# Performance work log

Hardware: AMD Instinct MI355X
Metric: run time of the kernel (lower is better)

Reference implementation:

```python
import jax, jax.numpy as jnp
import numpy as np

N_NODES = 50000
N_EDGES = 1600000
HID = 128
N_LAYERS = 3
N_GRAPHS = 64
LN_EPS = 1e-5


def setup_inputs() -> dict:
    key = jax.random.key(0)
    ks = jax.random.split(key, 8)
    x = jax.random.normal(ks[0], (N_NODES, HID), dtype=jnp.float32)
    edge_index = jax.random.randint(ks[1], (2, N_EDGES), 0, N_NODES)
    batch = jnp.sort(jax.random.randint(ks[2], (N_NODES,), 0, N_GRAPHS))
    s = 1.0 / np.sqrt(HID)
    Wn = jax.random.normal(ks[3], (N_LAYERS, HID, HID), dtype=jnp.float32) * s   # lin_l (neighbors)
    bn = jnp.zeros((N_LAYERS, HID), dtype=jnp.float32)                           # lin_l bias
    Wr = jax.random.normal(ks[4], (N_LAYERS, HID, HID), dtype=jnp.float32) * s   # lin_r (root), no bias
    gamma = jnp.ones((N_LAYERS, HID), dtype=jnp.float32)
    beta = jnp.zeros((N_LAYERS, HID), dtype=jnp.float32)
    return {"x": x, "Wn": Wn, "bn": bn, "Wr": Wr, "gamma": gamma, "beta": beta,
            "edge_index": edge_index, "batch": batch}


def _layer_norm(h, g, b):
    mu = jnp.mean(h, axis=-1, keepdims=True)
    var = jnp.mean((h - mu) ** 2, axis=-1, keepdims=True)
    return (h - mu) * jax.lax.rsqrt(var + LN_EPS) * g + b


def reference(x, Wn, bn, Wr, gamma, beta, edge_index, batch):
    src, dst = edge_index[0], edge_index[1]
    N = x.shape[0]
    # in-degree for mean aggregation (clamped to avoid div-by-zero for isolated nodes)
    deg = jax.ops.segment_sum(jnp.ones((src.shape[0],), x.dtype), dst, num_segments=N)
    inv_deg = 1.0 / jnp.maximum(deg, 1.0)
    for l in range(N_LAYERS):
        # SAGEConv: lin_l(mean_neighbor) + lin_r(x)
        agg = jax.ops.segment_sum(x[src], dst, num_segments=N) * inv_deg[:, None]
        h = agg @ Wn[l] + bn[l] + x @ Wr[l]
        h = _layer_norm(h, gamma[l], beta[l])
        x = jax.nn.relu(h)  # dropout is identity in eval mode
    node_emb = x
    cnt = jax.ops.segment_sum(jnp.ones((N,), x.dtype), batch, num_segments=N_GRAPHS)
    graph_emb = jax.ops.segment_sum(node_emb, batch, num_segments=N_GRAPHS) / jnp.maximum(cnt, 1.0)[:, None]
    return graph_emb, node_emb
```

## Files before the change

kernel.cpp:

```cpp
#include <hip/hip_runtime.h>

#define N_NODES 50000
#define N_EDGES 1600000
#define HID     128
#define N_GRAPHS 64

#define HB 200
#define EPB (N_EDGES / HB)
#define HWORDS 12500
#define NPP 12500
#define CWPP (NPP / 4)
#define NGRP 8
#define SPG (HB / NGRP)

#define WS_DEG   0u
#define WS_BSUM  50000u
#define WS_BOFF  50256u
#define WS_OFFS  50512u
#define WS_INVD  100512u
#define WS_CSR   150512u
#define WS_XB_B  1750512u
#define WS_GSUM  (WS_XB_B + 2500000u)
#define WS_XB_A  4950512u
#define WS_WP    8150512u
#define WS_END   8199664u

typedef __attribute__((ext_vector_type(8))) short short8;
typedef __attribute__((ext_vector_type(4))) float floatx4;

__device__ __forceinline__ float bf_lo(unsigned u) { return __uint_as_float(u << 16); }
__device__ __forceinline__ float bf_hi(unsigned u) { return __uint_as_float(u & 0xffff0000u); }
__device__ __forceinline__ unsigned bf_rn(float f) {
    unsigned u = __float_as_uint(f);
    unsigned r = ((u >> 16) & 1u) + 0x7fffu;
    return (u + r) >> 16;
}
__device__ __forceinline__ unsigned bf_pack(float lo, float hi) {
    return bf_rn(lo) | (bf_rn(hi) << 16);
}

__global__ __launch_bounds__(256) void k_prep(const float4* __restrict__ x, uint2* __restrict__ o,
                                              const float* __restrict__ Wn, const float* __restrict__ Wr,
                                              uint4* __restrict__ wp, const int* __restrict__ ei,
                                              unsigned* __restrict__ hist) {
    __shared__ unsigned sh[HWORDS];
    if (blockIdx.x < 6250) {
        int i = blockIdx.x * 256 + threadIdx.x;
        float4 v = x[i];
        uint2 r;
        r.x = bf_pack(v.x, v.y);
        r.y = bf_pack(v.z, v.w);
        o[i] = r;
    } else if (blockIdx.x < 6298) {
        int idx = (blockIdx.x - 6250) * 256 + threadIdx.x;
        int layer = idx >> 12;
        int rem = idx & 4095;
        int kb = rem >> 9;
        int n = (rem >> 2) & 127;
        int quad = rem & 3;
        float v[8];
#pragma unroll
        for (int j = 0; j < 8; j++) {
            int k = kb * 32 + quad * 8 + j;
            v[j] = (k < 128) ? Wn[layer * 16384 + k * 128 + n]
                             : Wr[layer * 16384 + (k - 128) * 128 + n];
        }
        uint4 r;
        r.x = bf_pack(v[0], v[1]);
        r.y = bf_pack(v[2], v[3]);
        r.z = bf_pack(v[4], v[5]);
        r.w = bf_pack(v[6], v[7]);
        wp[idx] = r;
    } else {
        const int hb = blockIdx.x - 6298;
        for (int i = threadIdx.x; i < HWORDS; i += 256) sh[i] = 0;
        __syncthreads();
        const int e0 = hb * EPB;
        for (int i = threadIdx.x; i < EPB; i += 256) {
            int d = __builtin_nontemporal_load(ei + N_EDGES + e0 + i);
            atomicAdd(&sh[d >> 2], 1u << ((d & 3) << 3));
        }
        __syncthreads();
        unsigned* hp = hist + (size_t)hb * HWORDS;
        for (int i = threadIdx.x; i < HWORDS; i += 256) hp[i] = sh[i];
    }
}


__global__ __launch_bounds__(256) void k_scanb1(unsigned* __restrict__ hist, unsigned* __restrict__ gsum) {
    int wb = blockIdx.x % 49;
    int g = blockIdx.x / 49;
    int w = wb * 256 + threadIdx.x;
    if (w >= HWORDS) return;
    size_t base = (size_t)(g * SPG) * HWORDS + w;
    unsigned run = 0;
#pragma unroll 5
    for (int b = 0; b < SPG; ++b) {
        unsigned u = hist[base + (size_t)b * HWORDS];
        hist[base + (size_t)b * HWORDS] = run;
        run += u;
    }
    gsum[(size_t)g * HWORDS + w] = run;
}

__global__ __launch_bounds__(256) void k_scanb2(unsigned* __restrict__ gsum, int* __restrict__ deg,
                                                int* __restrict__ bsum) {
    int w = blockIdx.x * 256 + threadIdx.x;
    int mysum = 0;
    if (w < HWORDS) {
        unsigned run = 0;
#pragma unroll
        for (int g = 0; g < NGRP; ++g) {
            unsigned u = gsum[(size_t)g * HWORDS + w];
            gsum[(size_t)g * HWORDS + w] = run;
            run += u;
        }
#pragma unroll
        for (int k = 0; k < 4; ++k) {
            int d = (int)((run >> (k << 3)) & 0xffu);
            deg[4 * w + k] = d;
            mysum += d;
        }
    }
    __shared__ int s[256];
    s[threadIdx.x] = mysum;
    __syncthreads();
    for (int d = 128; d > 0; d >>= 1) {
        if (threadIdx.x < d) s[threadIdx.x] += s[threadIdx.x + d];
        __syncthreads();
    }
    if (threadIdx.x == 0) bsum[blockIdx.x] = s[0];
}

__global__ __launch_bounds__(256) void k_offsets(const int* __restrict__ deg, const int* __restrict__ bsum,
                                                 int* __restrict__ offs, float* __restrict__ invdeg) {
    __shared__ int sb[64], sb0[64];
    __shared__ int s[256];
    int b = blockIdx.x, t = threadIdx.x;
    if (t < 64) {
        int v = (t < 49) ? bsum[t] : 0;
        sb[t] = v;
        sb0[t] = v;
    }
    __syncthreads();
    for (int d = 1; d < 64; d <<= 1) {
        int add = (t < 64 && t >= d) ? sb[t - d] : 0;
        __syncthreads();
        if (t < 64) sb[t] += add;
        __syncthreads();
    }
    int n0 = (b * 256 + t) * 4;
    int dl[4] = {0, 0, 0, 0};
#pragma unroll
    for (int k = 0; k < 4; ++k)
        if (n0 + k < N_NODES) dl[k] = deg[n0 + k];
    int v = dl[0] + dl[1] + dl[2] + dl[3];
    s[t] = v;
    __syncthreads();
    for (int dd = 1; dd < 256; dd <<= 1) {
        int add = (t >= dd) ? s[t - dd] : 0;
        __syncthreads();
        s[t] += add;
        __syncthreads();
    }
    int base = (sb[b] - sb0[b]) + s[t] - v;
#pragma unroll
    for (int k = 0; k < 4; ++k) {
        if (n0 + k < N_NODES) {
            offs[n0 + k] = base;
            invdeg[n0 + k] = 1.0f / fmaxf((float)dl[k], 1.0f);
            base += dl[k];
        }
    }
}

__global__ __launch_bounds__(256) void k_fill(const int* __restrict__ ei, const int* __restrict__ offs,
                                              const unsigned* __restrict__ hist,
                                              const unsigned* __restrict__ gpre,
                                              unsigned short* __restrict__ csr) {
    __shared__ unsigned scur[CWPP];
    const int pass = blockIdx.x & 3;
    const int b = blockIdx.x >> 2;
    const int nbase = pass * NPP;
    const unsigned* hb = hist + (size_t)b * HWORDS + pass * CWPP;
    const unsigned* gb = gpre + (size_t)(b / SPG) * HWORDS + pass * CWPP;
    for (int i = threadIdx.x; i < CWPP; i += 256) scur[i] = hb[i] + gb[i];
    __syncthreads();
    const int e0 = b * EPB;
    for (int i = threadIdx.x; i < EPB; i += 256) {
        int d = __builtin_nontemporal_load(ei + N_EDGES + e0 + i);
        unsigned rd = (unsigned)(d - nbase);
        if (rd < (unsigned)NPP) {
            int s = ei[e0 + i];
            int sh = (rd & 3) << 3;
            unsigned old = atomicAdd(&scur[rd >> 2], 1u << sh);
            unsigned rel = (old >> sh) & 0xffu;
            csr[offs[d] + (int)rel] = (unsigned short)s;
        }
    }
}

__global__ __launch_bounds__(256) void k_layer16(
        const uint4* __restrict__ xq, const unsigned short* __restrict__ csr,
        const int* __restrict__ offs, const int* __restrict__ deg,
        const float* __restrict__ invdeg, const uint4* __restrict__ wp,
        const float* __restrict__ bn, const float* __restrict__ gam,
        const float* __restrict__ bet, float* __restrict__ xout,
        unsigned* __restrict__ b16out, int write_f32) {
    __shared__ float H[16 * 132];
    uint4* A = (uint4*)H;

    const int t = threadIdx.x;
    const int wv = t >> 6;
    const int lane = t & 63;
    const int slot = lane >> 4;
    const int m = lane & 15;
    const int n0 = blockIdx.x * 16;
    const uint4* xm = xq + m;

    for (int i = 0; i < 4; ++i) {
        int node = __builtin_amdgcn_readfirstlane(n0 + wv * 4 + i);
        const int beg = offs[node];
        const int dn = deg[node];
        float a0 = 0.f, a1 = 0.f, a2 = 0.f, a3 = 0.f, a4 = 0.f, a5 = 0.f, a6 = 0.f, a7 = 0.f;
        int j = slot;
        for (; j + 32 <= dn; j += 32) {
            int s0 = csr[beg + j] << 4;
            int s1 = csr[beg + j + 4] << 4;
            int s2 = csr[beg + j + 8] << 4;
            int s3 = csr[beg + j + 12] << 4;
            int s4 = csr[beg + j + 16] << 4;
            int s5 = csr[beg + j + 20] << 4;
            int s6 = csr[beg + j + 24] << 4;
            int s7 = csr[beg + j + 28] << 4;
            uint4 u0 = xm[s0], u1 = xm[s1], u2 = xm[s2], u3 = xm[s3];
            uint4 u4 = xm[s4], u5 = xm[s5], u6 = xm[s6], u7 = xm[s7];
            a0 += ((bf_lo(u0.x) + bf_lo(u1.x)) + (bf_lo(u2.x) + bf_lo(u3.x))) + ((bf_lo(u4.x) + bf_lo(u5.x)) + (bf_lo(u6.x) + bf_lo(u7.x)));
            a1 += ((bf_hi(u0.x) + bf_hi(u1.x)) + (bf_hi(u2.x) + bf_hi(u3.x))) + ((bf_hi(u4.x) + bf_hi(u5.x)) + (bf_hi(u6.x) + bf_hi(u7.x)));
            a2 += ((bf_lo(u0.y) + bf_lo(u1.y)) + (bf_lo(u2.y) + bf_lo(u3.y))) + ((bf_lo(u4.y) + bf_lo(u5.y)) + (bf_lo(u6.y) + bf_lo(u7.y)));
            a3 += ((bf_hi(u0.y) + bf_hi(u1.y)) + (bf_hi(u2.y) + bf_hi(u3.y))) + ((bf_hi(u4.y) + bf_hi(u5.y)) + (bf_hi(u6.y) + bf_hi(u7.y)));
            a4 += ((bf_lo(u0.z) + bf_lo(u1.z)) + (bf_lo(u2.z) + bf_lo(u3.z))) + ((bf_lo(u4.z) + bf_lo(u5.z)) + (bf_lo(u6.z) + bf_lo(u7.z)));
            a5 += ((bf_hi(u0.z) + bf_hi(u1.z)) + (bf_hi(u2.z) + bf_hi(u3.z))) + ((bf_hi(u4.z) + bf_hi(u5.z)) + (bf_hi(u6.z) + bf_hi(u7.z)));
            a6 += ((bf_lo(u0.w) + bf_lo(u1.w)) + (bf_lo(u2.w) + bf_lo(u3.w))) + ((bf_lo(u4.w) + bf_lo(u5.w)) + (bf_lo(u6.w) + bf_lo(u7.w)));
            a7 += ((bf_hi(u0.w) + bf_hi(u1.w)) + (bf_hi(u2.w) + bf_hi(u3.w))) + ((bf_hi(u4.w) + bf_hi(u5.w)) + (bf_hi(u6.w) + bf_hi(u7.w)));
        }
        for (; j + 16 <= dn; j += 16) {
            int s0 = csr[beg + j] << 4;
            int s1 = csr[beg + j + 4] << 4;
            int s2 = csr[beg + j + 8] << 4;
            int s3 = csr[beg + j + 12] << 4;
            uint4 u0 = xm[s0], u1 = xm[s1], u2 = xm[s2], u3 = xm[s3];
            a0 += (bf_lo(u0.x) + bf_lo(u1.x)) + (bf_lo(u2.x) + bf_lo(u3.x));
            a1 += (bf_hi(u0.x) + bf_hi(u1.x)) + (bf_hi(u2.x) + bf_hi(u3.x));
            a2 += (bf_lo(u0.y) + bf_lo(u1.y)) + (bf_lo(u2.y) + bf_lo(u3.y));
            a3 += (bf_hi(u0.y) + bf_hi(u1.y)) + (bf_hi(u2.y) + bf_hi(u3.y));
            a4 += (bf_lo(u0.z) + bf_lo(u1.z)) + (bf_lo(u2.z) + bf_lo(u3.z));
            a5 += (bf_hi(u0.z) + bf_hi(u1.z)) + (bf_hi(u2.z) + bf_hi(u3.z));
            a6 += (bf_lo(u0.w) + bf_lo(u1.w)) + (bf_lo(u2.w) + bf_lo(u3.w));
            a7 += (bf_hi(u0.w) + bf_hi(u1.w)) + (bf_hi(u2.w) + bf_hi(u3.w));
        }
        for (; j < dn; j += 4) {
            uint4 u0 = xm[csr[beg + j] << 4];
            a0 += bf_lo(u0.x); a1 += bf_hi(u0.x);
            a2 += bf_lo(u0.y); a3 += bf_hi(u0.y);
            a4 += bf_lo(u0.z); a5 += bf_hi(u0.z);
            a6 += bf_lo(u0.w); a7 += bf_hi(u0.w);
        }
#pragma unroll
        for (int msk = 16; msk < 64; msk <<= 1) {
            a0 += __shfl_xor(a0, msk); a1 += __shfl_xor(a1, msk);
            a2 += __shfl_xor(a2, msk); a3 += __shfl_xor(a3, msk);
            a4 += __shfl_xor(a4, msk); a5 += __shfl_xor(a5, msk);
            a6 += __shfl_xor(a6, msk); a7 += __shfl_xor(a7, msk);
        }
        if (slot == 0) {
            float id = invdeg[node];
            uint4 r;
            r.x = bf_pack(a0 * id, a1 * id);
            r.y = bf_pack(a2 * id, a3 * id);
            r.z = bf_pack(a4 * id, a5 * id);
            r.w = bf_pack(a6 * id, a7 * id);
            A[(wv * 4 + i) * 17 + m] = r;
        }
    }
    __syncthreads();

    const int quad = lane >> 4;
    const int nl = lane & 15;
    const int nb = wv * 32;
    floatx4 acc0 = {0.f, 0.f, 0.f, 0.f}, acc1 = acc0;
#pragma unroll
    for (int kb = 0; kb < 8; ++kb) {
        uint4 av = (kb < 4) ? A[nl * 17 + kb * 4 + quad]
                            : xq[(n0 + nl) * 16 + (kb - 4) * 4 + quad];
        uint4 b0 = wp[(kb * 128 + nb + nl) * 4 + quad];
        uint4 b1 = wp[(kb * 128 + nb + 16 + nl) * 4 + quad];
        short8 as = *(short8*)&av;
        short8 b0s = *(short8*)&b0, b1s = *(short8*)&b1;
        acc0 = __builtin_amdgcn_mfma_f32_16x16x32_bf16(as, b0s, acc0, 0, 0, 0);
        acc1 = __builtin_amdgcn_mfma_f32_16x16x32_bf16(as, b1s, acc1, 0, 0, 0);
    }
    __syncthreads();

    float bn0 = bn[nb + nl];
    float bn1 = bn[nb + 16 + nl];
#pragma unroll
    for (int reg = 0; reg < 4; ++reg) {
        int rr = quad * 4 + reg;
        H[rr * 132 + nb + nl] = acc0[reg] + bn0;
        H[rr * 132 + nb + 16 + nl] = acc1[reg] + bn1;
    }
    __syncthreads();

    const int row = t >> 4;
    const int sub = t & 15;
    const float* hr = &H[row * 132 + sub * 8];
    float v[8];
    float s = 0.f, s2 = 0.f;
#pragma unroll
    for (int i = 0; i < 8; i++) {
        v[i] = hr[i];
        s += v[i];
        s2 += v[i] * v[i];
    }
#pragma unroll
    for (int msk = 1; msk < 16; msk <<= 1) {
        s += __shfl_xor(s, msk);
        s2 += __shfl_xor(s2, msk);
    }
    float mean = s * (1.f / 128.f);
    float var = s2 * (1.f / 128.f) - mean * mean;
    float rstd = rsqrtf(var + 1e-5f);
    const int gr = n0 + row;
    const int cb = sub * 8;
    float o[8];
#pragma unroll
    for (int i = 0; i < 8; i++)
        o[i] = fmaxf((v[i] - mean) * rstd * gam[cb + i] + bet[cb + i], 0.f);
    if (write_f32) {
        *(float4*)&xout[(size_t)gr * HID + cb] = *(float4*)&o[0];
        *(float4*)&xout[(size_t)gr * HID + cb + 4] = *(float4*)&o[4];
    }
    unsigned p[4];
#pragma unroll
    for (int i = 0; i < 4; i++) p[i] = bf_pack(o[2 * i], o[2 * i + 1]);
    *(uint4*)&b16out[(size_t)gr * 64 + (cb >> 1)] = *(uint4*)&p[0];
}


__global__ __launch_bounds__(1024) void k_pool1(const unsigned* __restrict__ xb,
                                                const int* __restrict__ batch,
                                                float* __restrict__ partial, int* __restrict__ cnt) {
    const int bid = blockIdx.x;
    const int g = bid >> 2;
    const int part = bid & 3;
    __shared__ int s_beg, s_end;
    if (threadIdx.x == 0) {
        int lo = 0, hi = N_NODES;
        while (lo < hi) { int mid = (lo + hi) >> 1; if (batch[mid] < g) lo = mid + 1; else hi = mid; }
        s_beg = lo;
        lo = 0; hi = N_NODES;
        while (lo < hi) { int mid = (lo + hi) >> 1; if (batch[mid] < g + 1) lo = mid + 1; else hi = mid; }
        s_end = lo;
    }
    __syncthreads();
    const int beg = s_beg, end = s_end;
    const int w = threadIdx.x & 63;
    const int q = threadIdx.x >> 6;
    float ax = 0.f, ay = 0.f;
    for (int r = beg + part * 16 + q; r < end; r += 64) {
        unsigned u = __builtin_nontemporal_load(xb + (size_t)r * 64 + w);
        ax += bf_lo(u);
        ay += bf_hi(u);
    }
    __shared__ float sx[16][64], sy[16][64];
    sx[q][w] = ax;
    sy[q][w] = ay;
    __syncthreads();
    if (q == 0) {
        float tx = 0.f, ty = 0.f;
#pragma unroll
        for (int i = 0; i < 16; i++) { tx += sx[i][w]; ty += sy[i][w]; }
        float2 r;
        r.x = tx;
        r.y = ty;
        *(float2*)&partial[(size_t)bid * 128 + w * 2] = r;
    }
    if (part == 0 && threadIdx.x == 0) cnt[g] = end - beg;
}

__global__ __launch_bounds__(256) void k_pool2(const float* __restrict__ partial,
                                               const int* __restrict__ cnt,
                                               float* __restrict__ out) {
    int idx = blockIdx.x * 256 + threadIdx.x;
    int g = idx >> 7;
    float s = partial[(size_t)(g * 4 + 0) * 128 + (idx & 127)]
            + partial[(size_t)(g * 4 + 1) * 128 + (idx & 127)]
            + partial[(size_t)(g * 4 + 2) * 128 + (idx & 127)]
            + partial[(size_t)(g * 4 + 3) * 128 + (idx & 127)];
    out[idx] = s / fmaxf((float)cnt[g], 1.f);
}

extern "C" void kernel_launch(void* const* d_in, const int* in_sizes, int n_in,
                              void* d_out, int out_size, void* d_ws, size_t ws_size,
                              hipStream_t stream) {
    const float* x0 = (const float*)d_in[0];
    const float* Wn = (const float*)d_in[1];
    const float* bn = (const float*)d_in[2];
    const float* Wr = (const float*)d_in[3];
    const float* gam = (const float*)d_in[4];
    const float* bet = (const float*)d_in[5];
    const int* ei = (const int*)d_in[6];
    const int* batch = (const int*)d_in[7];

    float* out = (float*)d_out;
    float* node_out = out + N_GRAPHS * HID;

    unsigned* ws = (unsigned*)d_ws;
    int* deg = (int*)(ws + WS_DEG);
    int* bsum = (int*)(ws + WS_BSUM);
    int* offs = (int*)(ws + WS_OFFS);
    float* invdeg = (float*)(ws + WS_INVD);
    unsigned short* csr = (unsigned short*)(ws + WS_CSR);
    unsigned* hist = ws + WS_XB_B;
    unsigned* gsum = ws + WS_GSUM;
    unsigned* xa = ws + WS_XB_A;
    unsigned* xbb = ws + WS_XB_B;
    uint4* wp = (uint4*)(ws + WS_WP);
    float* partial = (float*)(ws + WS_CSR);
    int* cnt = (int*)(ws + WS_CSR + 256 * 128);

    k_prep<<<6498, 256, 0, stream>>>((const float4*)x0, (uint2*)xa, Wn, Wr, wp, ei, hist);
    k_scanb1<<<NGRP * 49, 256, 0, stream>>>(hist, gsum);
    k_scanb2<<<49, 256, 0, stream>>>(gsum, deg, bsum);
    k_offsets<<<49, 256, 0, stream>>>(deg, bsum, offs, invdeg);
    k_fill<<<HB * 4, 256, 0, stream>>>(ei, offs, hist, gsum, csr);

    const int lb = N_NODES / 16;

    for (int l = 0; l < 3; ++l) {
        const unsigned* xin = (l & 1) ? xbb : xa;
        unsigned* xout16 = (l & 1) ? xa : xbb;
        k_layer16<<<lb, 256, 0, stream>>>((const uint4*)xin, csr, offs, deg, invdeg,
                                          wp + (size_t)l * 4096, bn + (size_t)l * HID,
                                          gam + (size_t)l * HID, bet + (size_t)l * HID,
                                          node_out, xout16, l == 2 ? 1 : 0);
    }

    k_pool1<<<N_GRAPHS * 4, 1024, 0, stream>>>(xbb, batch, partial, cnt);
    k_pool2<<<32, 256, 0, stream>>>(partial, cnt, out);
}
```

Before: 449.7 us.

## Sort CSR neighbors by source quarter and gather in block-synchronized phases

The histogram/fill pipeline now buckets each node's neighbor list by which quarter of the node range the source falls in, so CSR segments are grouped by source region. The layer kernel assigns one node per 16-lane slot (instead of a whole wave per node) and gathers the four source-quarter segments in lockstep separated by __syncthreads, aiming to keep concurrently gathered rows within a smaller, cache-resident slice of the feature matrix. In exchange, the histogram kernel reads sources for every edge four times, the fill kernel has fewer blocks with larger shared memory, and per-slot parallelism means more load imbalance across nodes with different degrees.

```diff
diff --git a/kernel.cpp b/kernel.cpp
--- a/kernel.cpp
+++ b/kernel.cpp
@@ -5,8 +5,11 @@
 #define HID     128
 #define N_GRAPHS 64
 
-#define HB 200
-#define EPB (N_EDGES / HB)
+#define NQ 4
+#define QN (N_NODES / NQ)
+#define SUBS 50
+#define EPB (N_EDGES / SUBS)
+#define HB (NQ * SUBS)
 #define HWORDS 12500
 #define NPP 12500
 #define CWPP (NPP / 4)
@@ -19,8 +22,8 @@
 #define WS_OFFS  50512u
 #define WS_INVD  100512u
 #define WS_CSR   150512u
+#define WS_GSUM  950512u
 #define WS_XB_B  1750512u
-#define WS_GSUM  (WS_XB_B + 2500000u)
 #define WS_XB_A  4950512u
 #define WS_WP    8150512u
 #define WS_END   8199664u
@@ -41,9 +44,7 @@
 
 __global__ __launch_bounds__(256) void k_prep(const float4* __restrict__ x, uint2* __restrict__ o,
                                               const float* __restrict__ Wn, const float* __restrict__ Wr,
-                                              uint4* __restrict__ wp, const int* __restrict__ ei,
-                                              unsigned* __restrict__ hist) {
-    __shared__ unsigned sh[HWORDS];
+                                              uint4* __restrict__ wp) {
     if (blockIdx.x < 6250) {
         int i = blockIdx.x * 256 + threadIdx.x;
         float4 v = x[i];
@@ -51,7 +52,7 @@
         r.x = bf_pack(v.x, v.y);
         r.y = bf_pack(v.z, v.w);
         o[i] = r;
-    } else if (blockIdx.x < 6298) {
+    } else {
         int idx = (blockIdx.x - 6250) * 256 + threadIdx.x;
         int layer = idx >> 12;
         int rem = idx & 4095;
@@ -71,21 +72,28 @@
         r.z = bf_pack(v[4], v[5]);
         r.w = bf_pack(v[6], v[7]);
         wp[idx] = r;
-    } else {
-        const int hb = blockIdx.x - 6298;
-        for (int i = threadIdx.x; i < HWORDS; i += 256) sh[i] = 0;
-        __syncthreads();
-        const int e0 = hb * EPB;
-        for (int i = threadIdx.x; i < EPB; i += 256) {
+    }
+}
+
+
+__global__ __launch_bounds__(256) void k_hist(const int* __restrict__ ei, unsigned* __restrict__ hist) {
+    __shared__ unsigned sh[HWORDS];
+    const int s = blockIdx.x >> 2;
+    const int q = blockIdx.x & 3;
+    for (int i = threadIdx.x; i < HWORDS; i += 256) sh[i] = 0;
+    __syncthreads();
+    const int e0 = s * EPB;
+    for (int i = threadIdx.x; i < EPB; i += 256) {
+        int src = ei[e0 + i];
+        if (src / QN == q) {
             int d = __builtin_nontemporal_load(ei + N_EDGES + e0 + i);
             atomicAdd(&sh[d >> 2], 1u << ((d & 3) << 3));
         }
-        __syncthreads();
-        unsigned* hp = hist + (size_t)hb * HWORDS;
-        for (int i = threadIdx.x; i < HWORDS; i += 256) hp[i] = sh[i];
-    }
-}
-
+    }
+    __syncthreads();
+    unsigned* hp = hist + (size_t)(q * SUBS + s) * HWORDS;
+    for (int i = threadIdx.x; i < HWORDS; i += 256) hp[i] = sh[i];
+}
 
 __global__ __launch_bounds__(256) void k_scanb1(unsigned* __restrict__ hist, unsigned* __restrict__ gsum) {
     int wb = blockIdx.x % 49;
@@ -178,24 +186,29 @@
                                               const unsigned* __restrict__ hist,
                                               const unsigned* __restrict__ gpre,
                                               unsigned short* __restrict__ csr) {
-    __shared__ unsigned scur[CWPP];
-    const int pass = blockIdx.x & 3;
-    const int b = blockIdx.x >> 2;
-    const int nbase = pass * NPP;
-    const unsigned* hb = hist + (size_t)b * HWORDS + pass * CWPP;
-    const unsigned* gb = gpre + (size_t)(b / SPG) * HWORDS + pass * CWPP;
-    for (int i = threadIdx.x; i < CWPP; i += 256) scur[i] = hb[i] + gb[i];
-    __syncthreads();
-    const int e0 = b * EPB;
+    __shared__ unsigned scur[NQ * CWPP];
+    const int s = blockIdx.x >> 2;
+    const int p = blockIdx.x & 3;
+    const int nbase = p * NPP;
+    for (int i = threadIdx.x; i < NQ * CWPP; i += 256) {
+        int q = i / CWPP;
+        int w = i - q * CWPP;
+        int g = 2 * q + (s >= SPG);
+        scur[i] = hist[(size_t)(q * SUBS + s) * HWORDS + p * CWPP + w]
+                + gpre[(size_t)g * HWORDS + p * CWPP + w];
+    }
+    __syncthreads();
+    const int e0 = s * EPB;
     for (int i = threadIdx.x; i < EPB; i += 256) {
         int d = __builtin_nontemporal_load(ei + N_EDGES + e0 + i);
         unsigned rd = (unsigned)(d - nbase);
         if (rd < (unsigned)NPP) {
-            int s = ei[e0 + i];
+            int src = ei[e0 + i];
+            int q = src / QN;
             int sh = (rd & 3) << 3;
-            unsigned old = atomicAdd(&scur[rd >> 2], 1u << sh);
+            unsigned old = atomicAdd(&scur[q * CWPP + (int)(rd >> 2)], 1u << sh);
             unsigned rel = (old >> sh) & 0xffu;
-            csr[offs[d] + (int)rel] = (unsigned short)s;
+            csr[offs[d] + (int)rel] = (unsigned short)src;
         }
     }
 }
@@ -203,10 +216,10 @@
 __global__ __launch_bounds__(256) void k_layer16(
         const uint4* __restrict__ xq, const unsigned short* __restrict__ csr,
         const int* __restrict__ offs, const int* __restrict__ deg,
-        const float* __restrict__ invdeg, const uint4* __restrict__ wp,
-        const float* __restrict__ bn, const float* __restrict__ gam,
-        const float* __restrict__ bet, float* __restrict__ xout,
-        unsigned* __restrict__ b16out, int write_f32) {
+        const unsigned* __restrict__ gpre, const float* __restrict__ invdeg,
+        const uint4* __restrict__ wp, const float* __restrict__ bn,
+        const float* __restrict__ gam, const float* __restrict__ bet,
+        float* __restrict__ xout, unsigned* __restrict__ b16out, int write_f32) {
     __shared__ float H[16 * 132];
     uint4* A = (uint4*)H;
 
@@ -218,70 +231,61 @@
     const int n0 = blockIdx.x * 16;
     const uint4* xm = xq + m;
 
-    for (int i = 0; i < 4; ++i) {
-        int node = __builtin_amdgcn_readfirstlane(n0 + wv * 4 + i);
-        const int beg = offs[node];
-        const int dn = deg[node];
-        float a0 = 0.f, a1 = 0.f, a2 = 0.f, a3 = 0.f, a4 = 0.f, a5 = 0.f, a6 = 0.f, a7 = 0.f;
-        int j = slot;
-        for (; j + 32 <= dn; j += 32) {
-            int s0 = csr[beg + j] << 4;
-            int s1 = csr[beg + j + 4] << 4;
-            int s2 = csr[beg + j + 8] << 4;
-            int s3 = csr[beg + j + 12] << 4;
-            int s4 = csr[beg + j + 16] << 4;
-            int s5 = csr[beg + j + 20] << 4;
-            int s6 = csr[beg + j + 24] << 4;
-            int s7 = csr[beg + j + 28] << 4;
-            uint4 u0 = xm[s0], u1 = xm[s1], u2 = xm[s2], u3 = xm[s3];
-            uint4 u4 = xm[s4], u5 = xm[s5], u6 = xm[s6], u7 = xm[s7];
-            a0 += ((bf_lo(u0.x) + bf_lo(u1.x)) + (bf_lo(u2.x) + bf_lo(u3.x))) + ((bf_lo(u4.x) + bf_lo(u5.x)) + (bf_lo(u6.x) + bf_lo(u7.x)));
-            a1 += ((bf_hi(u0.x) + bf_hi(u1.x)) + (bf_hi(u2.x) + bf_hi(u3.x))) + ((bf_hi(u4.x) + bf_hi(u5.x)) + (bf_hi(u6.x) + bf_hi(u7.x)));
-            a2 += ((bf_lo(u0.y) + bf_lo(u1.y)) + (bf_lo(u2.y) + bf_lo(u3.y))) + ((bf_lo(u4.y) + bf_lo(u5.y)) + (bf_lo(u6.y) + bf_lo(u7.y)));
-            a3 += ((bf_hi(u0.y) + bf_hi(u1.y)) + (bf_hi(u2.y) + bf_hi(u3.y))) + ((bf_hi(u4.y) + bf_hi(u5.y)) + (bf_hi(u6.y) + bf_hi(u7.y)));
-            a4 += ((bf_lo(u0.z) + bf_lo(u1.z)) + (bf_lo(u2.z) + bf_lo(u3.z))) + ((bf_lo(u4.z) + bf_lo(u5.z)) + (bf_lo(u6.z) + bf_lo(u7.z)));
-            a5 += ((bf_hi(u0.z) + bf_hi(u1.z)) + (bf_hi(u2.z) + bf_hi(u3.z))) + ((bf_hi(u4.z) + bf_hi(u5.z)) + (bf_hi(u6.z) + bf_hi(u7.z)));
-            a6 += ((bf_lo(u0.w) + bf_lo(u1.w)) + (bf_lo(u2.w) + bf_lo(u3.w))) + ((bf_lo(u4.w) + bf_lo(u5.w)) + (bf_lo(u6.w) + bf_lo(u7.w)));
-            a7 += ((bf_hi(u0.w) + bf_hi(u1.w)) + (bf_hi(u2.w) + bf_hi(u3.w))) + ((bf_hi(u4.w) + bf_hi(u5.w)) + (bf_hi(u6.w) + bf_hi(u7.w)));
-        }
-        for (; j + 16 <= dn; j += 16) {
-            int s0 = csr[beg + j] << 4;
-            int s1 = csr[beg + j + 4] << 4;
-            int s2 = csr[beg + j + 8] << 4;
-            int s3 = csr[beg + j + 12] << 4;
-            uint4 u0 = xm[s0], u1 = xm[s1], u2 = xm[s2], u3 = xm[s3];
-            a0 += (bf_lo(u0.x) + bf_lo(u1.x)) + (bf_lo(u2.x) + bf_lo(u3.x));
-            a1 += (bf_hi(u0.x) + bf_hi(u1.x)) + (bf_hi(u2.x) + bf_hi(u3.x));
-            a2 += (bf_lo(u0.y) + bf_lo(u1.y)) + (bf_lo(u2.y) + bf_lo(u3.y));
-            a3 += (bf_hi(u0.y) + bf_hi(u1.y)) + (bf_hi(u2.y) + bf_hi(u3.y));
-            a4 += (bf_lo(u0.z) + bf_lo(u1.z)) + (bf_lo(u2.z) + bf_lo(u3.z));
-            a5 += (bf_hi(u0.z) + bf_hi(u1.z)) + (bf_hi(u2.z) + bf_hi(u3.z));
-            a6 += (bf_lo(u0.w) + bf_lo(u1.w)) + (bf_lo(u2.w) + bf_lo(u3.w));
-            a7 += (bf_hi(u0.w) + bf_hi(u1.w)) + (bf_hi(u2.w) + bf_hi(u3.w));
-        }
-        for (; j < dn; j += 4) {
-            uint4 u0 = xm[csr[beg + j] << 4];
-            a0 += bf_lo(u0.x); a1 += bf_hi(u0.x);
-            a2 += bf_lo(u0.y); a3 += bf_hi(u0.y);
-            a4 += bf_lo(u0.z); a5 += bf_hi(u0.z);
-            a6 += bf_lo(u0.w); a7 += bf_hi(u0.w);
-        }
-#pragma unroll
-        for (int msk = 16; msk < 64; msk <<= 1) {
-            a0 += __shfl_xor(a0, msk); a1 += __shfl_xor(a1, msk);
-            a2 += __shfl_xor(a2, msk); a3 += __shfl_xor(a3, msk);
-            a4 += __shfl_xor(a4, msk); a5 += __shfl_xor(a5, msk);
-            a6 += __shfl_xor(a6, msk); a7 += __shfl_xor(a7, msk);
-        }
-        if (slot == 0) {
-            float id = invdeg[node];
-            uint4 r;
-            r.x = bf_pack(a0 * id, a1 * id);
-            r.y = bf_pack(a2 * id, a3 * id);
-            r.z = bf_pack(a4 * id, a5 * id);
-            r.w = bf_pack(a6 * id, a7 * id);
-            A[(wv * 4 + i) * 17 + m] = r;
-        }
+    const int node = n0 + wv * 4 + slot;
+    const int beg = offs[node];
+    const int dtot = deg[node];
+    const int wrd = node >> 2;
+    const int sh8 = (node & 3) << 3;
+    const int q1 = (gpre[2 * HWORDS + wrd] >> sh8) & 0xff;
+    const int q2 = (gpre[4 * HWORDS + wrd] >> sh8) & 0xff;
+    const int q3 = (gpre[6 * HWORDS + wrd] >> sh8) & 0xff;
+
+    float a0 = 0.f, a1 = 0.f, a2 = 0.f, a3 = 0.f, a4 = 0.f, a5 = 0.f, a6 = 0.f, a7 = 0.f;
+
+#define SEG_GATHER(JB, JE)                                                        \
+    {                                                                             \
+        int j = (JB);                                                             \
+        const int e = (JE);                                                       \
+        for (; j + 4 <= e; j += 4) {                                              \
+            int s0 = csr[j] << 4;                                                 \
+            int s1 = csr[j + 1] << 4;                                             \
+            int s2 = csr[j + 2] << 4;                                             \
+            int s3 = csr[j + 3] << 4;                                             \
+            uint4 u0 = xm[s0], u1 = xm[s1], u2 = xm[s2], u3 = xm[s3];             \
+            a0 += (bf_lo(u0.x) + bf_lo(u1.x)) + (bf_lo(u2.x) + bf_lo(u3.x));      \
+            a1 += (bf_hi(u0.x) + bf_hi(u1.x)) + (bf_hi(u2.x) + bf_hi(u3.x));      \
+            a2 += (bf_lo(u0.y) + bf_lo(u1.y)) + (bf_lo(u2.y) + bf_lo(u3.y));      \
+            a3 += (bf_hi(u0.y) + bf_hi(u1.y)) + (bf_hi(u2.y) + bf_hi(u3.y));      \
+            a4 += (bf_lo(u0.z) + bf_lo(u1.z)) + (bf_lo(u2.z) + bf_lo(u3.z));      \
+            a5 += (bf_hi(u0.z) + bf_hi(u1.z)) + (bf_hi(u2.z) + bf_hi(u3.z));      \
+            a6 += (bf_lo(u0.w) + bf_lo(u1.w)) + (bf_lo(u2.w) + bf_lo(u3.w));      \
+            a7 += (bf_hi(u0.w) + bf_hi(u1.w)) + (bf_hi(u2.w) + bf_hi(u3.w));      \
+        }                                                                         \
+        for (; j < e; ++j) {                                                      \
+            uint4 u0 = xm[csr[j] << 4];                                           \
+            a0 += bf_lo(u0.x); a1 += bf_hi(u0.x);                                 \
+            a2 += bf_lo(u0.y); a3 += bf_hi(u0.y);                                 \
+            a4 += bf_lo(u0.z); a5 += bf_hi(u0.z);                                 \
+            a6 += bf_lo(u0.w); a7 += bf_hi(u0.w);                                 \
+        }                                                                         \
+    }
+
+    SEG_GATHER(beg, beg + q1)
+    __syncthreads();
+    SEG_GATHER(beg + q1, beg + q2)
+    __syncthreads();
+    SEG_GATHER(beg + q2, beg + q3)
+    __syncthreads();
+    SEG_GATHER(beg + q3, beg + dtot)
+
+    {
+        float id = invdeg[node];
+        uint4 r;
+        r.x = bf_pack(a0 * id, a1 * id);
+        r.y = bf_pack(a2 * id, a3 * id);
+        r.z = bf_pack(a4 * id, a5 * id);
+        r.w = bf_pack(a6 * id, a7 * id);
+        A[(wv * 4 + slot) * 17 + m] = r;
     }
     __syncthreads();
 
@@ -422,26 +426,27 @@
     int* offs = (int*)(ws + WS_OFFS);
     float* invdeg = (float*)(ws + WS_INVD);
     unsigned short* csr = (unsigned short*)(ws + WS_CSR);
+    unsigned* gsum = ws + WS_GSUM;
     unsigned* hist = ws + WS_XB_B;
-    unsigned* gsum = ws + WS_GSUM;
     unsigned* xa = ws + WS_XB_A;
     unsigned* xbb = ws + WS_XB_B;
     uint4* wp = (uint4*)(ws + WS_WP);
     float* partial = (float*)(ws + WS_CSR);
     int* cnt = (int*)(ws + WS_CSR + 256 * 128);
 
-    k_prep<<<6498, 256, 0, stream>>>((const float4*)x0, (uint2*)xa, Wn, Wr, wp, ei, hist);
+    k_prep<<<6298, 256, 0, stream>>>((const float4*)x0, (uint2*)xa, Wn, Wr, wp);
+    k_hist<<<SUBS * NQ, 256, 0, stream>>>(ei, hist);
     k_scanb1<<<NGRP * 49, 256, 0, stream>>>(hist, gsum);
     k_scanb2<<<49, 256, 0, stream>>>(gsum, deg, bsum);
     k_offsets<<<49, 256, 0, stream>>>(deg, bsum, offs, invdeg);
-    k_fill<<<HB * 4, 256, 0, stream>>>(ei, offs, hist, gsum, csr);
+    k_fill<<<SUBS * 4, 256, 0, stream>>>(ei, offs, hist, gsum, csr);
 
     const int lb = N_NODES / 16;
 
     for (int l = 0; l < 3; ++l) {
         const unsigned* xin = (l & 1) ? xbb : xa;
         unsigned* xout16 = (l & 1) ? xa : xbb;
-        k_layer16<<<lb, 256, 0, stream>>>((const uint4*)xin, csr, offs, deg, invdeg,
+        k_layer16<<<lb, 256, 0, stream>>>((const uint4*)xin, csr, offs, deg, gsum, invdeg,
                                           wp + (size_t)l * 4096, bn + (size_t)l * HID,
                                           gam + (size_t)l * HID, bet + (size_t)l * HID,
                                           node_out, xout16, l == 2 ? 1 : 0);
```

Measured after the change: 571.6 us. 1.27x slower.
